# Kernel optimization log

Hardware: AMD Instinct MI355X
Metric: run time of the kernel (lower is better)

Reference implementation:

```python
import jax, jax.numpy as jnp
import numpy as np

E = 200000      # number of edge tokens
M = 3200000     # number of e2e attention pairs
IN_DIM = 64
EMBED = 64
H = 8
D = EMBED // H


def setup_inputs() -> dict:
    key = jax.random.key(0)
    ks = jax.random.split(key, 12)
    s = 1.0 / np.sqrt(IN_DIM)
    inp = {
        "edge_features": jax.random.normal(ks[0], (E, IN_DIM), dtype=jnp.float32),
        "e2e": jax.random.randint(ks[1], (2, M), 0, E, dtype=jnp.int32),
        "attn_bias": jax.random.normal(ks[2], (M, H), dtype=jnp.float32),
        "Wq": jax.random.uniform(ks[3], (IN_DIM, EMBED), jnp.float32, -s, s),
        "bq": jax.random.uniform(ks[4], (EMBED,), jnp.float32, -s, s),
        "Wk": jax.random.uniform(ks[5], (IN_DIM, EMBED), jnp.float32, -s, s),
        "bk": jax.random.uniform(ks[6], (EMBED,), jnp.float32, -s, s),
        "Wv": jax.random.uniform(ks[7], (IN_DIM, EMBED), jnp.float32, -s, s),
        "bv": jax.random.uniform(ks[8], (EMBED,), jnp.float32, -s, s),
        "Wo": jax.random.uniform(ks[9], (EMBED, EMBED), jnp.float32, -s, s),
        "bo": jax.random.uniform(ks[10], (EMBED,), jnp.float32, -s, s),
    }
    return inp


def _segment_softmax(logits, index, num_segments):
    # logits: (M, H) grouped by index (dst edge id)
    seg_max = jax.ops.segment_max(logits, index, num_segments=num_segments)
    seg_max = jnp.where(jnp.isfinite(seg_max), seg_max, 0.0)  # empty segments
    ex = jnp.exp(logits - seg_max[index])
    seg_sum = jax.ops.segment_sum(ex, index, num_segments=num_segments)
    return ex / (seg_sum[index] + 1e-16)


def reference(edge_features, e2e, attn_bias, Wq, bq, Wk, bk, Wv, bv, Wo, bo):
    src_e, dst_e = e2e[0], e2e[1]
    scale = D ** (-0.5)
    q = (edge_features @ Wq + bq).reshape(E, H, D)
    k = (edge_features @ Wk + bk).reshape(E, H, D)
    v = (edge_features @ Wv + bv).reshape(E, H, D)
    q_dst = q[dst_e]                       # (M, H, D) gather
    k_src = k[src_e]                       # (M, H, D) gather
    logits = jnp.sum(q_dst * k_src, axis=-1) * scale   # (M, H)
    logits = logits + attn_bias
    attn = _segment_softmax(logits, dst_e, E)          # (M, H)
    msg = v[src_e] * attn[..., None]                   # (M, H, D)
    out = jax.ops.segment_sum(msg, dst_e, num_segments=E)  # (E, H, D)
    out = out.reshape(E, EMBED)
    return out @ Wo + bo
```

## Files before the change

kernel.cpp:

```cpp
#include <hip/hip_runtime.h>

#define E_N 200000
#define M_N 3200000
#define SCAN_CHUNK 2048
#define NB1 98

#define NBUCK 782
#define NCHUNK 1000
#define CH 3200
#define BLEN (NBUCK * NCHUNK)
#define NB2 382
#define NP 4
#define SMAX 8192

typedef __attribute__((ext_vector_type(8))) short bf16x8;
typedef __attribute__((ext_vector_type(4))) float f32x4;
typedef __attribute__((ext_vector_type(8))) _Float16 f16x8;

__device__ __forceinline__ short f2bf(float f) {
    union { float f; unsigned u; } x; x.f = f;
    unsigned r = x.u + 0x7fffu + ((x.u >> 16) & 1u);
    return (short)(r >> 16);
}

__global__ __launch_bounds__(256) void qkv_mfma(
    const float* __restrict__ x,
    const float* __restrict__ Wq, const float* __restrict__ bq,
    const float* __restrict__ Wk, const float* __restrict__ bk,
    const float* __restrict__ Wv, const float* __restrict__ bv,
    float* __restrict__ q, _Float16* __restrict__ k, _Float16* __restrict__ v)
{
    const int w    = threadIdx.x >> 6;
    const int lane = threadIdx.x & 63;
    const int quad = lane >> 4;
    const int m    = lane & 15;

    bf16x8 Bq[4][2], Bk[4][2], Bv[4][2];
    float  bqv[4], bkv[4], bvv[4];
    #pragma unroll
    for (int ct = 0; ct < 4; ct++) {
        int cc = ct * 16 + m;
        bqv[ct] = bq[cc]; bkv[ct] = bk[cc]; bvv[ct] = bv[cc];
        #pragma unroll
        for (int kb = 0; kb < 2; kb++) {
            #pragma unroll
            for (int j = 0; j < 8; j++) {
                int kk = kb * 32 + quad * 8 + j;
                Bq[ct][kb][j] = f2bf(Wq[kk * 64 + cc]);
                Bk[ct][kb][j] = f2bf(Wk[kk * 64 + cc]);
                Bv[ct][kb][j] = f2bf(Wv[kk * 64 + cc]);
            }
        }
    }

    for (int row0 = blockIdx.x * 64 + w * 16; row0 < E_N; row0 += gridDim.x * 64) {
        const float* xr = x + (long long)(row0 + m) * 64 + quad * 8;
        bf16x8 A[2];
        #pragma unroll
        for (int kb = 0; kb < 2; kb++) {
            float4 p0 = *(const float4*)(xr + kb * 32);
            float4 p1 = *(const float4*)(xr + kb * 32 + 4);
            A[kb][0] = f2bf(p0.x); A[kb][1] = f2bf(p0.y);
            A[kb][2] = f2bf(p0.z); A[kb][3] = f2bf(p0.w);
            A[kb][4] = f2bf(p1.x); A[kb][5] = f2bf(p1.y);
            A[kb][6] = f2bf(p1.z); A[kb][7] = f2bf(p1.w);
        }

        #pragma unroll
        for (int ct = 0; ct < 4; ct++) {
            f32x4 aq = {bqv[ct], bqv[ct], bqv[ct], bqv[ct]};
            f32x4 ak = {bkv[ct], bkv[ct], bkv[ct], bkv[ct]};
            f32x4 av = {bvv[ct], bvv[ct], bvv[ct], bvv[ct]};
            aq = __builtin_amdgcn_mfma_f32_16x16x32_bf16(A[0], Bq[ct][0], aq, 0, 0, 0);
            aq = __builtin_amdgcn_mfma_f32_16x16x32_bf16(A[1], Bq[ct][1], aq, 0, 0, 0);
            ak = __builtin_amdgcn_mfma_f32_16x16x32_bf16(A[0], Bk[ct][0], ak, 0, 0, 0);
            ak = __builtin_amdgcn_mfma_f32_16x16x32_bf16(A[1], Bk[ct][1], ak, 0, 0, 0);
            av = __builtin_amdgcn_mfma_f32_16x16x32_bf16(A[0], Bv[ct][0], av, 0, 0, 0);
            av = __builtin_amdgcn_mfma_f32_16x16x32_bf16(A[1], Bv[ct][1], av, 0, 0, 0);
            #pragma unroll
            for (int i = 0; i < 4; i++) {
                long long off = (long long)(row0 + quad * 4 + i) * 64 + ct * 16 + m;
                q[off] = aq[i];
                k[off] = (_Float16)ak[i];
                v[off] = (_Float16)av[i];
            }
        }
    }
}

__global__ __launch_bounds__(256) void hist_kernel(
    const int* __restrict__ e2e, int* __restrict__ counts)
{
    int m4 = (blockIdx.x * 256 + threadIdx.x) * 4;
    if (m4 < M_N) {
        int4 d = *(const int4*)(e2e + M_N + m4);
        atomicAdd(&counts[d.x], 1);
        atomicAdd(&counts[d.y], 1);
        atomicAdd(&counts[d.z], 1);
        atomicAdd(&counts[d.w], 1);
    }
}

__global__ __launch_bounds__(256) void scan1_kernel(
    const int* __restrict__ counts, int* __restrict__ cursor,
    int* __restrict__ blocksums, int len)
{
    __shared__ int s[256];
    const int t = threadIdx.x;
    const int base = blockIdx.x * SCAN_CHUNK + t * 8;

    int vals[8];
    int tot = 0;
    #pragma unroll
    for (int j = 0; j < 8; j++) {
        int idx = base + j;
        vals[j] = (idx < len) ? counts[idx] : 0;
        tot += vals[j];
    }
    s[t] = tot;
    __syncthreads();
    for (int off = 1; off < 256; off <<= 1) {
        int add = (t >= off) ? s[t - off] : 0;
        __syncthreads();
        s[t] += add;
        __syncthreads();
    }
    int excl = (t == 0) ? 0 : s[t - 1];
    if (t == 255) blocksums[blockIdx.x] = s[255];

    int run = excl;
    #pragma unroll
    for (int j = 0; j < 8; j++) {
        int idx = base + j;
        if (idx < len) cursor[idx] = run;
        run += vals[j];
    }
}

__global__ __launch_bounds__(256) void scan2_kernel(
    const int* __restrict__ blocksums, int* __restrict__ blockoff, int nb)
{
    __shared__ int s[256];
    const int t = threadIdx.x;
    int vals[4];
    int tot = 0;
    #pragma unroll
    for (int u = 0; u < 4; u++) {
        int idx = t * 4 + u;
        vals[u] = (idx < nb) ? blocksums[idx] : 0;
        tot += vals[u];
    }
    s[t] = tot;
    __syncthreads();
    for (int off = 1; off < 256; off <<= 1) {
        int add = (t >= off) ? s[t - off] : 0;
        __syncthreads();
        s[t] += add;
        __syncthreads();
    }
    int run = (t == 0) ? 0 : s[t - 1];
    #pragma unroll
    for (int u = 0; u < 4; u++) {
        int idx = t * 4 + u;
        if (idx < nb) blockoff[idx] = run;
        run += vals[u];
    }
}

__global__ __launch_bounds__(1024) void bhist_kernel(
    const int* __restrict__ e2e, int* __restrict__ bcnt)
{
    __shared__ int lc[NBUCK];
    const int c = blockIdx.x;
    for (int i = threadIdx.x; i < NBUCK; i += 1024) lc[i] = 0;
    __syncthreads();
    const int m0 = c * CH;
    for (int i = threadIdx.x * 4; i < CH; i += 4096) {
        int4 d = *(const int4*)(e2e + M_N + m0 + i);
        atomicAdd(&lc[d.x >> 8], 1);
        atomicAdd(&lc[d.y >> 8], 1);
        atomicAdd(&lc[d.z >> 8], 1);
        atomicAdd(&lc[d.w >> 8], 1);
    }
    __syncthreads();
    for (int i = threadIdx.x; i < NBUCK; i += 1024) bcnt[i * NCHUNK + c] = lc[i];
}

__global__ __launch_bounds__(1024, 4) void scatter_bucket(
    const int* __restrict__ e2e, const float* __restrict__ bias,
    const int* __restrict__ bcur0, const int* __restrict__ boff2,
    int* __restrict__ meta, _Float16* __restrict__ bias_s)
{
    __shared__ int gbase[NBUCK];
    __shared__ unsigned short bk[CH];
    __shared__ char pool[CH * 16] __attribute__((aligned(16)));
    int*   cnt     = (int*)pool;
    int*   s       = (int*)(pool + 4096);
    f16x8* stage_b = (f16x8*)pool;
    int*   stage_m = (int*)pool;

    const int c = blockIdx.x;
    const int t = threadIdx.x;
    const int m0 = c * CH;

    for (int b = t; b < NBUCK; b += 1024) {
        cnt[b] = 0;
        int idx = b * NCHUNK + c;
        gbase[b] = bcur0[idx] + boff2[idx >> 11];
    }
    __syncthreads();

    int   mt[NP];
    int   pk[NP];
    f16x8 bb[NP];
    #pragma unroll
    for (int r = 0; r < NP; r++) {
        int i = t + r * 1024;
        pk[r] = -1;
        if (i < CH) {
            int m = m0 + i;
            int dst = e2e[M_N + m];
            int src = e2e[m];
            int b = dst >> 8;
            pk[r] = b << 12;
            mt[r] = ((dst & 255) << 18) | src;
            float4 b0 = *(const float4*)(bias + (long long)m * 8);
            float4 b1 = *(const float4*)(bias + (long long)m * 8 + 4);
            f16x8 xx;
            xx[0] = (_Float16)b0.x; xx[1] = (_Float16)b0.y;
            xx[2] = (_Float16)b0.z; xx[3] = (_Float16)b0.w;
            xx[4] = (_Float16)b1.x; xx[5] = (_Float16)b1.y;
            xx[6] = (_Float16)b1.z; xx[7] = (_Float16)b1.w;
            bb[r] = xx;
            atomicAdd(&cnt[b], 1);
        }
    }
    __syncthreads();

    int v = (t < NBUCK) ? cnt[t] : 0;
    s[t] = v;
    __syncthreads();
    for (int off = 1; off < 1024; off <<= 1) {
        int add = (t >= off) ? s[t - off] : 0;
        __syncthreads();
        s[t] += add;
        __syncthreads();
    }
    if (t < NBUCK) {
        int excl = (t == 0) ? 0 : s[t - 1];
        gbase[t] -= excl;
        cnt[t] = excl;
    }
    __syncthreads();

    #pragma unroll
    for (int r = 0; r < NP; r++) {
        if (pk[r] >= 0) {
            int b = pk[r] >> 12;
            int j = atomicAdd(&cnt[b], 1);
            pk[r] = (b << 12) | j;
        }
    }
    __syncthreads();

    #pragma unroll
    for (int r = 0; r < NP; r++) {
        if (pk[r] >= 0) {
            int j = pk[r] & 4095;
            stage_b[j] = bb[r];
            bk[j] = (unsigned short)(pk[r] >> 12);
        }
    }
    __syncthreads();
    for (int j = t; j < CH; j += 1024) {
        int slot = gbase[bk[j]] + j;
        *(f16x8*)(bias_s + (long long)slot * 8) = stage_b[j];
    }
    __syncthreads();

    #pragma unroll
    for (int r = 0; r < NP; r++) {
        if (pk[r] >= 0) stage_m[pk[r] & 4095] = mt[r];
    }
    __syncthreads();
    for (int j = t; j < CH; j += 1024) {
        meta[gbase[bk[j]] + j] = stage_m[j];
    }
}

__global__ __launch_bounds__(512, 2) void bucket_permute(
    const int* __restrict__ cursor, const int* __restrict__ boff,
    int* __restrict__ meta, _Float16* __restrict__ bias_s)
{
    __shared__ int smeta[SMAX];
    __shared__ int cnt[256];
    __shared__ int scn[256];
    const int b = blockIdx.x;
    const int t = threadIdx.x;
    const int d0 = b << 8;
    const int bs = cursor[d0] + boff[d0 >> 11];
    const int d1 = d0 + 256;
    const int be = (d1 < E_N) ? (cursor[d1] + boff[d1 >> 11]) : M_N;
    int n = be - bs;
    if (n > SMAX) n = SMAX;

    if (t < 256) cnt[t] = 0;
    __syncthreads();
    #pragma unroll
    for (int r = 0; r < SMAX / 512; r++) {
        int i = t + r * 512;
        if (i < n) {
            int mm = meta[bs + i];
            smeta[i] = mm;
            atomicAdd(&cnt[mm >> 18], 1);
        }
    }
    __syncthreads();
    if (t < 256) scn[t] = cnt[t];
    __syncthreads();
    for (int off = 1; off < 256; off <<= 1) {
        int v = 0;
        if (t < 256 && t >= off) v = scn[t - off];
        __syncthreads();
        if (t < 256) scn[t] += v;
        __syncthreads();
    }
    if (t < 256) cnt[t] = scn[t] - cnt[t];
    __syncthreads();

    int    pos[SMAX / 512];
    f16x8  bb[SMAX / 512];
    #pragma unroll
    for (int r = 0; r < SMAX / 512; r++) {
        int i = t + r * 512;
        if (i < n) {
            int mm = smeta[i];
            pos[r] = bs + atomicAdd(&cnt[mm >> 18], 1);
            bb[r]  = *(const f16x8*)(bias_s + (long long)(bs + i) * 8);
        }
    }
    __syncthreads();
    #pragma unroll
    for (int r = 0; r < SMAX / 512; r++) {
        int i = t + r * 512;
        if (i < n) {
            meta[pos[r]] = smeta[i] & 0x3FFFF;
            *(f16x8*)(bias_s + (long long)pos[r] * 8) = bb[r];
        }
    }
}

__global__ __launch_bounds__(256) void aggregate_kernel(
    const _Float16* __restrict__ k, const _Float16* __restrict__ v,
    const _Float16* __restrict__ bias_s,
    const int* __restrict__ counts, const int* __restrict__ cursor,
    const int* __restrict__ blockoff,
    const int* __restrict__ sorted,
    float* __restrict__ qmsg)
{
    const int wid  = threadIdx.x >> 6;
    const int lane = threadIdx.x & 63;
    const int ps   = lane >> 3;
    const int t    = lane & 7;

    for (int e = blockIdx.x * 4 + wid; e < E_N; e += gridDim.x * 4) {
        float qv = qmsg[(long long)e * 64 + lane];

        float qs[8];
        #pragma unroll
        for (int j = 0; j < 8; j++) qs[j] = __shfl(qv, t * 8 + j, 64);

        int start = cursor[e] + blockoff[e >> 11];
        int cnt   = counts[e];
        int end   = start + cnt;

        float acc = 0.0f, wsum = 0.0f;
        for (int i = start; i < end; i += 8) {
            int idx = i + ps;
            bool valid = idx < end;
            int src = valid ? sorted[idx] : 0;
            float bs = valid ? (float)bias_s[(long long)idx * 8 + t] : 0.0f;

            f16x8 kk = *(const f16x8*)(k + (long long)src * 64 + t * 8);
            float dot = 0.0f;
            #pragma unroll
            for (int j = 0; j < 8; j++) dot = fmaf(qs[j], (float)kk[j], dot);

            float w = valid ? __expf(fmaf(dot, 0.35355339059327373f, bs)) : 0.0f;

            int   srcj[8];
            float wj[8];
            #pragma unroll
            for (int j = 0; j < 8; j++) {
                srcj[j] = __shfl(src, j * 8, 64);
                wj[j]   = __shfl(w, j * 8 + ps, 64);
            }
            #pragma unroll
            for (int j = 0; j < 8; j++) {
                float vv = (float)v[(long long)srcj[j] * 64 + lane];
                acc  += wj[j] * vv;
                wsum += wj[j];
            }
        }
        qmsg[(long long)e * 64 + lane] = acc / (wsum + 1e-16f);
    }
}

__global__ __launch_bounds__(256) void out_mfma(
    const float* __restrict__ Wo, const float* __restrict__ bo,
    float* __restrict__ out)
{
    const int w    = threadIdx.x >> 6;
    const int lane = threadIdx.x & 63;
    const int quad = lane >> 4;
    const int m    = lane & 15;

    bf16x8 B[4][2];
    float  bov[4];
    #pragma unroll
    for (int ct = 0; ct < 4; ct++) {
        int cc = ct * 16 + m;
        bov[ct] = bo[cc];
        #pragma unroll
        for (int kb = 0; kb < 2; kb++) {
            #pragma unroll
            for (int j = 0; j < 8; j++) {
                int kk = kb * 32 + quad * 8 + j;
                B[ct][kb][j] = f2bf(Wo[kk * 64 + cc]);
            }
        }
    }

    for (int row0 = blockIdx.x * 64 + w * 16; row0 < E_N; row0 += gridDim.x * 64) {
        const float* xr = out + (long long)(row0 + m) * 64 + quad * 8;
        bf16x8 A[2];
        #pragma unroll
        for (int kb = 0; kb < 2; kb++) {
            float4 p0 = *(const float4*)(xr + kb * 32);
            float4 p1 = *(const float4*)(xr + kb * 32 + 4);
            A[kb][0] = f2bf(p0.x); A[kb][1] = f2bf(p0.y);
            A[kb][2] = f2bf(p0.z); A[kb][3] = f2bf(p0.w);
            A[kb][4] = f2bf(p1.x); A[kb][5] = f2bf(p1.y);
            A[kb][6] = f2bf(p1.z); A[kb][7] = f2bf(p1.w);
        }

        f32x4 acc[4];
        #pragma unroll
        for (int ct = 0; ct < 4; ct++) {
            acc[ct] = (f32x4){bov[ct], bov[ct], bov[ct], bov[ct]};
            acc[ct] = __builtin_amdgcn_mfma_f32_16x16x32_bf16(A[0], B[ct][0], acc[ct], 0, 0, 0);
            acc[ct] = __builtin_amdgcn_mfma_f32_16x16x32_bf16(A[1], B[ct][1], acc[ct], 0, 0, 0);
        }
        #pragma unroll
        for (int ct = 0; ct < 4; ct++) {
            #pragma unroll
            for (int i = 0; i < 4; i++) {
                out[(long long)(row0 + quad * 4 + i) * 64 + ct * 16 + m] = acc[ct][i];
            }
        }
    }
}

extern "C" void kernel_launch(void* const* d_in, const int* in_sizes, int n_in,
                              void* d_out, int out_size, void* d_ws, size_t ws_size,
                              hipStream_t stream) {
    const float* x    = (const float*)d_in[0];
    const int*   e2e  = (const int*)  d_in[1];
    const float* bias = (const float*)d_in[2];
    const float* Wq   = (const float*)d_in[3];
    const float* bq   = (const float*)d_in[4];
    const float* Wk   = (const float*)d_in[5];
    const float* bk   = (const float*)d_in[6];
    const float* Wv   = (const float*)d_in[7];
    const float* bv   = (const float*)d_in[8];
    const float* Wo   = (const float*)d_in[9];
    const float* bo   = (const float*)d_in[10];
    float* out = (float*)d_out;

    _Float16* kh     = (_Float16*)d_ws;
    _Float16* vh     = kh + (long long)E_N * 64;
    int*      counts = (int*)(vh + (long long)E_N * 64);
    int*      cursor = counts + E_N;
    int*      bsum   = cursor + E_N;
    int*      boff   = bsum + 512;
    int*      sorted = boff + 512;
    _Float16* bias_s = (_Float16*)(sorted + M_N);
    int*      bcnt   = (int*)(bias_s + (long long)M_N * 8);
    int*      bsum2  = bcnt + BLEN;
    int*      boff2  = bsum2 + 512;

    hipMemsetAsync(counts, 0, (size_t)E_N * sizeof(int), stream);

    qkv_mfma<<<640, 256, 0, stream>>>(x, Wq, bq, Wk, bk, Wv, bv, out, kh, vh);

    hist_kernel<<<M_N / 1024, 256, 0, stream>>>(e2e, counts);
    scan1_kernel<<<NB1, 256, 0, stream>>>(counts, cursor, bsum, E_N);
    scan2_kernel<<<1, 256, 0, stream>>>(bsum, boff, NB1);

    bhist_kernel<<<NCHUNK, 1024, 0, stream>>>(e2e, bcnt);
    scan1_kernel<<<NB2, 256, 0, stream>>>(bcnt, bcnt, bsum2, BLEN);
    scan2_kernel<<<1, 256, 0, stream>>>(bsum2, boff2, NB2);

    scatter_bucket<<<NCHUNK, 1024, 0, stream>>>(e2e, bias, bcnt, boff2,
                                                sorted, bias_s);
    bucket_permute<<<NBUCK, 512, 0, stream>>>(cursor, boff, sorted, bias_s);

    aggregate_kernel<<<8192, 256, 0, stream>>>(kh, vh, bias_s, counts, cursor,
                                               boff, sorted, out);

    out_mfma<<<640, 256, 0, stream>>>(Wo, bo, out);
}
```

Before: 663.8 us.

## Restructure aggregate loop to per-slot V accumulation with 2x unroll and xor reduction

The aggregation kernel changes from broadcasting weights and src indices with shuffles, followed by per-lane scalar V gathers, to having each lane-slot gather a full 8-wide V vector for its own pair and accumulate locally. Each iteration handles 16 pairs instead of 8, which raises memory-level parallelism, and a cross-slot xor-shuffle reduction runs at the end before vectorized stores. The aim is to remove the 16 shuffles per iteration and the scattered 2-byte V loads. In exchange it adds register pressure and wasted work on segments shorter than 16 pairs.

```diff
diff --git a/kernel.cpp b/kernel.cpp
--- a/kernel.cpp
+++ b/kernel.cpp
@@ -365,7 +365,6 @@
 
     for (int e = blockIdx.x * 4 + wid; e < E_N; e += gridDim.x * 4) {
         float qv = qmsg[(long long)e * 64 + lane];
-
         float qs[8];
         #pragma unroll
         for (int j = 0; j < 8; j++) qs[j] = __shfl(qv, t * 8 + j, 64);
@@ -374,35 +373,57 @@
         int cnt   = counts[e];
         int end   = start + cnt;
 
-        float acc = 0.0f, wsum = 0.0f;
-        for (int i = start; i < end; i += 8) {
-            int idx = i + ps;
-            bool valid = idx < end;
-            int src = valid ? sorted[idx] : 0;
-            float bs = valid ? (float)bias_s[(long long)idx * 8 + t] : 0.0f;
-
-            f16x8 kk = *(const f16x8*)(k + (long long)src * 64 + t * 8);
-            float dot = 0.0f;
-            #pragma unroll
-            for (int j = 0; j < 8; j++) dot = fmaf(qs[j], (float)kk[j], dot);
-
-            float w = valid ? __expf(fmaf(dot, 0.35355339059327373f, bs)) : 0.0f;
-
-            int   srcj[8];
-            float wj[8];
+        float acc[8] = {0.f,0.f,0.f,0.f,0.f,0.f,0.f,0.f};
+        float ws = 0.0f;
+
+        for (int i = start; i < end; i += 16) {
+            int iA = i + ps;
+            int iB = i + 8 + ps;
+            bool vA = iA < end, vB = iB < end;
+            int cA = vA ? iA : start;
+            int cB = vB ? iB : start;
+            int sA = sorted[cA];
+            int sB = sorted[cB];
+            float bA = (float)bias_s[(long long)cA * 8 + t];
+            float bB = (float)bias_s[(long long)cB * 8 + t];
+            f16x8 kA = *(const f16x8*)(k + (long long)sA * 64 + t * 8);
+            f16x8 kB = *(const f16x8*)(k + (long long)sB * 64 + t * 8);
+            f16x8 vA8 = *(const f16x8*)(v + (long long)sA * 64 + t * 8);
+            f16x8 vB8 = *(const f16x8*)(v + (long long)sB * 64 + t * 8);
+
+            float dA = 0.0f, dB = 0.0f;
             #pragma unroll
             for (int j = 0; j < 8; j++) {
-                srcj[j] = __shfl(src, j * 8, 64);
-                wj[j]   = __shfl(w, j * 8 + ps, 64);
+                dA = fmaf(qs[j], (float)kA[j], dA);
+                dB = fmaf(qs[j], (float)kB[j], dB);
             }
+            float wA = vA ? __expf(fmaf(dA, 0.35355339059327373f, bA)) : 0.0f;
+            float wB = vB ? __expf(fmaf(dB, 0.35355339059327373f, bB)) : 0.0f;
+            ws += wA + wB;
             #pragma unroll
             for (int j = 0; j < 8; j++) {
-                float vv = (float)v[(long long)srcj[j] * 64 + lane];
-                acc  += wj[j] * vv;
-                wsum += wj[j];
+                acc[j] = fmaf(wA, (float)vA8[j], acc[j]);
+                acc[j] = fmaf(wB, (float)vB8[j], acc[j]);
             }
         }
-        qmsg[(long long)e * 64 + lane] = acc / (wsum + 1e-16f);
+
+        #pragma unroll
+        for (int st = 8; st <= 32; st <<= 1) {
+            #pragma unroll
+            for (int j = 0; j < 8; j++) acc[j] += __shfl_xor(acc[j], st, 64);
+            ws += __shfl_xor(ws, st, 64);
+        }
+
+        if (ps == 0) {
+            float inv = 1.0f / (ws + 1e-16f);
+            float4 o0, o1;
+            o0.x = acc[0]*inv; o0.y = acc[1]*inv;
+            o0.z = acc[2]*inv; o0.w = acc[3]*inv;
+            o1.x = acc[4]*inv; o1.y = acc[5]*inv;
+            o1.z = acc[6]*inv; o1.w = acc[7]*inv;
+            *(float4*)(qmsg + (long long)e * 64 + t * 8)     = o0;
+            *(float4*)(qmsg + (long long)e * 64 + t * 8 + 4) = o1;
+        }
     }
 }
 
```

New measurement: 652.1 us. No clear change (-1.8%).
